# Performance work log

Measured on AMD Instinct MI355X. Metric: run time of the kernel, lower is better.

The kernel has to match this reference:

```python
import jax, jax.numpy as jnp
import numpy as np

# Llama-7B-like config with CPSVD split projections
B, S, H = 1, 1024, 4096
NH, HD = 32, 128          # num_heads, head_dim
RANK = 1024               # SVD rank per projection
NCOL = 512                # exactly-kept columns per projection
NSVD = H - NCOL           # SVD-compressed columns
ROPE_BASE = 10000.0
WSCALE = 0.02


def setup_inputs() -> dict:
    key = jax.random.key(0)
    ks = jax.random.split(key, 16)
    hidden_states = jax.random.normal(ks[0], (B, S, H), jnp.float32)
    # causal additive mask (large negative above diagonal)
    causal = jnp.triu(jnp.full((S, S), -1e9, jnp.float32), k=1)
    attention_mask = jnp.broadcast_to(causal, (B, 1, S, S))
    position_ids = jnp.broadcast_to(jnp.arange(S, dtype=jnp.int32), (B, S))
    # disjoint partition of the 4096 input columns: 512 kept, 3584 SVD'd
    col_idx = jnp.arange(0, H, H // NCOL, dtype=jnp.int32)          # [512]
    keep = np.ones(H, dtype=bool); keep[np.asarray(col_idx)] = False
    svd_idx = jnp.asarray(np.nonzero(keep)[0], dtype=jnp.int32)      # [3584]
    # per-projection weights (torch Linear convention: [out, in])
    def w(k, shape):
        return jax.random.normal(k, shape, jnp.float32) * WSCALE
    inp = dict(hidden_states=hidden_states, attention_mask=attention_mask,
               position_ids=position_ids, col_idx=col_idx, svd_idx=svd_idx)
    names = ['q', 'k', 'v', 'o']
    for i, p in enumerate(names):
        inp[f'{p}_v_w'] = w(ks[1 + 3 * i], (RANK, NSVD))   # v_proj: n_svd -> rank
        inp[f'{p}_u_w'] = w(ks[2 + 3 * i], (H, RANK))      # u_proj: rank -> hidden
        inp[f'{p}_col_w'] = w(ks[3 + 3 * i], (H, NCOL))    # col: n_col -> hidden
    return inp


def _split_proj(x, svd_idx, col_idx, v_w, u_w, col_w):
    # x: [B,S,H] -> gather + low-rank (V then U) + exact-column matmul, added
    x_svd = x[..., svd_idx]                                  # [B,S,NSVD]
    x_col = x[..., col_idx]                                  # [B,S,NCOL]
    low = jnp.einsum('bsr,hr->bsh', jnp.einsum('bsn,rn->bsr', x_svd, v_w), u_w)
    return low + jnp.einsum('bsc,hc->bsh', x_col, col_w)     # [B,S,H]


def _rotate_half(x):
    x1, x2 = x[..., : HD // 2], x[..., HD // 2 :]
    return jnp.concatenate((-x2, x1), axis=-1)


def reference(hidden_states, attention_mask, position_ids, col_idx, svd_idx,
              q_v_w, q_u_w, q_col_w, k_v_w, k_u_w, k_col_w,
              v_v_w, v_u_w, v_col_w, o_v_w, o_u_w, o_col_w):
    bsz, q_len, _ = hidden_states.shape

    def heads(t):  # [B,S,H] -> [B,NH,S,HD]
        return t.reshape(bsz, q_len, NH, HD).transpose(0, 2, 1, 3)

    q = heads(_split_proj(hidden_states, svd_idx, col_idx, q_v_w, q_u_w, q_col_w))
    k = heads(_split_proj(hidden_states, svd_idx, col_idx, k_v_w, k_u_w, k_col_w))
    v = heads(_split_proj(hidden_states, svd_idx, col_idx, v_v_w, v_u_w, v_col_w))

    # rotary embedding: direct indexed read of cos/sin tables
    inv_freq = 1.0 / (ROPE_BASE ** (jnp.arange(0, HD, 2, dtype=jnp.float32) / HD))
    ang = jnp.arange(q_len, dtype=jnp.float32)[:, None] * inv_freq[None, :]  # [S,HD/2]
    emb = jnp.concatenate((ang, ang), axis=-1)                               # [S,HD]
    cos = jnp.cos(emb)[position_ids][:, None, :, :]                          # [B,1,S,HD]
    sin = jnp.sin(emb)[position_ids][:, None, :, :]
    q = q * cos + _rotate_half(q) * sin
    k = k * cos + _rotate_half(k) * sin

    scale = 1.0 / jnp.sqrt(jnp.float32(HD))
    attn = jnp.einsum('bhqd,bhkd->bhqk', q, k) * scale
    attn = attn + attention_mask
    attn = jnp.maximum(attn, jnp.finfo(attn.dtype).min)
    attn = jax.nn.softmax(attn.astype(jnp.float32), axis=-1).astype(q.dtype)
    out = jnp.einsum('bhqk,bhkd->bhqd', attn, v)             # [B,NH,S,HD]
    out = out.transpose(0, 2, 1, 3).reshape(bsz, q_len, NH * HD)
    out = _split_proj(out, svd_idx, col_idx, o_v_w, o_u_w, o_col_w)
    return out
```

## Files before the change

### kernel.cpp

```cpp
#include <hip/hip_runtime.h>

typedef __attribute__((ext_vector_type(8))) short short8;
typedef __attribute__((ext_vector_type(4))) float f32x4;
typedef unsigned short u16;
typedef unsigned int u32;
typedef unsigned long long u64;

__device__ __forceinline__ u16 f2bf(float f) {
  u32 u = __builtin_bit_cast(u32, f);
  u32 r = u + 0x7FFFu + ((u >> 16) & 1u);
  return (u16)(r >> 16);
}
__device__ __forceinline__ float bf2f(u16 h) {
  u32 u = ((u32)h) << 16;
  return __builtin_bit_cast(float, u);
}

__device__ __forceinline__ void gload16(const void* g, void* l) {
  __builtin_amdgcn_global_load_lds(
      (const __attribute__((address_space(1))) void*)(u64)g,
      (__attribute__((address_space(3))) void*)(u32)(u64)l,
      16, 0, 0);
}

__global__ void convertk(const float* __restrict__ src, u16* __restrict__ dst, int n4) {
  int i = blockIdx.x * blockDim.x + threadIdx.x;
  if (i >= n4) return;
  float4 v = ((const float4*)src)[i];
  ushort4 o;
  o.x = f2bf(v.x); o.y = f2bf(v.y); o.z = f2bf(v.z); o.w = f2bf(v.w);
  ((ushort4*)dst)[i] = o;
}

__global__ void rowcat(const float* __restrict__ u, const float* __restrict__ c,
                       u16* __restrict__ dst) {
  int i = blockIdx.x * blockDim.x + threadIdx.x;
  if (i >= 4096 * 384) return;
  int r = i / 384, c4 = i % 384;
  float4 v = (c4 < 256) ? ((const float4*)(u + (long)r * 1024))[c4]
                        : ((const float4*)(c + (long)r * 512))[c4 - 256];
  ushort4 o;
  o.x = f2bf(v.x); o.y = f2bf(v.y); o.z = f2bf(v.z); o.w = f2bf(v.w);
  ((ushort4*)(dst + (long)r * 1536))[c4] = o;
}

__global__ void gather_in(const float* __restrict__ hid, const int* __restrict__ svd,
                          const int* __restrict__ col, u16* __restrict__ Xs,
                          u16* __restrict__ X2) {
  int s = blockIdx.x;
  const float* row = hid + (long)s * 4096;
  for (int j = threadIdx.x; j < 3584; j += blockDim.x)
    Xs[(long)s * 3584 + j] = f2bf(row[svd[j]]);
  for (int c = threadIdx.x; c < 512; c += blockDim.x) {
    u16 v = f2bf(row[col[c]]);
    X2[(long)s * 1536 + 1024 + c] = v;
    X2[1024L * 1536 + (long)s * 1536 + 1024 + c] = v;
    X2[2 * 1024L * 1536 + (long)s * 1536 + 1024 + c] = v;
  }
}

__global__ void gather_o(const u16* __restrict__ Ao, const int* __restrict__ svd,
                         const int* __restrict__ col, u16* __restrict__ Xso,
                         u16* __restrict__ X2o) {
  int s = blockIdx.x;
  const u16* row = Ao + (long)s * 4096;
  for (int j = threadIdx.x; j < 3584; j += blockDim.x)
    Xso[(long)s * 3584 + j] = row[svd[j]];
  for (int c = threadIdx.x; c < 512; c += blockDim.x)
    X2o[(long)s * 1536 + 1024 + c] = row[col[c]];
}

__global__ void rope_k(const u16* __restrict__ P, u16* __restrict__ dst, float scale) {
  int tid = blockIdx.x * blockDim.x + threadIdx.x;
  int d = tid & 127, s = (tid >> 7) & 1023, h = tid >> 17;
  float x = bf2f(P[(long)s * 4096 + h * 128 + d]);
  int dp = (d < 64) ? d + 64 : d - 64;
  float xp = bf2f(P[(long)s * 4096 + h * 128 + dp]);
  float rot = (d < 64) ? -xp : xp;
  int fi = d & 63;
  float inv = exp2f(-(float)fi * 0.20762050593046013f);
  float ang = (float)s * inv;
  float sn, cs;
  sincosf(ang, &sn, &cs);
  dst[((long)h * 1024 + s) * 128 + d] = f2bf((x * cs + rot * sn) * scale);
}

__global__ void vtrans(const u16* __restrict__ P, u16* __restrict__ Vt) {
  __shared__ u16 t[64][65];
  int h = blockIdx.z, d0 = blockIdx.y * 64, s0 = blockIdx.x * 64;
  int c = threadIdx.x & 63, r0 = threadIdx.x >> 6;
  for (int r = r0; r < 64; r += 4)
    t[r][c] = P[(long)(s0 + r) * 4096 + h * 128 + d0 + c];
  __syncthreads();
  for (int r = r0; r < 64; r += 4)
    Vt[(long)(h * 128 + d0 + r) * 1024 + s0 + c] = t[c][r];
}

template <int FOUT>
__global__ __launch_bounds__(256) void gemm_nt(const u16* __restrict__ A,
                                               const u16* __restrict__ B,
                                               void* __restrict__ Cv, int K, int ldc,
                                               long sAz, long sBz, long sCz) {
  __shared__ __align__(16) u16 As[128 * 64];
  __shared__ __align__(16) u16 Bs[128 * 64];
  const int tid = threadIdx.x;
  const int w = tid >> 6, lane = tid & 63;
  const int wr = w >> 1, wc = w & 1;
  const int lr = lane & 15, lk = lane >> 4;
  const u16* Ab = A + (long)blockIdx.z * sAz + (long)blockIdx.y * 128 * K;
  const u16* Bb = B + (long)blockIdx.z * sBz + (long)blockIdx.x * 128 * K;
  const int srow = w * 8 + (lane >> 3);
  const int scol = (lane & 7) * 8;

  f32x4 acc[4][4] = {};

  for (int k0 = 0; k0 < K; k0 += 64) {
#pragma unroll
    for (int i = 0; i < 4; ++i) {
      gload16(Ab + (long)(i * 32 + srow) * K + k0 + scol, &As[i * 2048 + w * 512]);
      gload16(Bb + (long)(i * 32 + srow) * K + k0 + scol, &Bs[i * 2048 + w * 512]);
    }
    __syncthreads();
#pragma unroll
    for (int kk = 0; kk < 2; ++kk) {
      short8 af[4], bf[4];
#pragma unroll
      for (int m = 0; m < 4; ++m) {
        af[m] = *(const short8*)&As[(wr * 64 + m * 16 + lr) * 64 + kk * 32 + lk * 8];
      }
#pragma unroll
      for (int n = 0; n < 4; ++n) {
        bf[n] = *(const short8*)&Bs[(wc * 64 + n * 16 + lr) * 64 + kk * 32 + lk * 8];
      }
#pragma unroll
      for (int m = 0; m < 4; ++m) {
#pragma unroll
        for (int n = 0; n < 4; ++n) {
          acc[m][n] = __builtin_amdgcn_mfma_f32_16x16x32_bf16(af[m], bf[n], acc[m][n], 0, 0, 0);
        }
      }
    }
    __syncthreads();
  }

  const long crow = (long)blockIdx.y * 128 + wr * 64 + lk * 4;
  const long ccol = (long)blockIdx.x * 128 + wc * 64 + lr;
  if constexpr (FOUT == 0) {
    u16* C = (u16*)Cv + (long)blockIdx.z * sCz;
#pragma unroll
    for (int m = 0; m < 4; ++m) {
#pragma unroll
      for (int n = 0; n < 4; ++n) {
#pragma unroll
        for (int j = 0; j < 4; ++j)
          C[(crow + m * 16 + j) * ldc + ccol + n * 16] = f2bf(acc[m][n][j]);
      }
    }
  } else {
    float* C = (float*)Cv + (long)blockIdx.z * sCz;
#pragma unroll
    for (int m = 0; m < 4; ++m) {
#pragma unroll
      for (int n = 0; n < 4; ++n) {
#pragma unroll
        for (int j = 0; j < 4; ++j)
          C[(crow + m * 16 + j) * ldc + ccol + n * 16] = acc[m][n][j];
      }
    }
  }
}

__global__ __launch_bounds__(256) void attn_k(const u16* __restrict__ Qh,
                                              const u16* __restrict__ Kh,
                                              const u16* __restrict__ Vt,
                                              u16* __restrict__ Ao) {
  const int qt = 15 - blockIdx.x;
  const int h = blockIdx.y;
  const int w = threadIdx.x >> 6, lane = threadIdx.x & 63;
  const int q0 = qt * 64 + w * 16;
  const int lr = lane & 15, lk = lane >> 4;

  __shared__ __align__(16) u16 Plds[4][16][72];

  short8 qf[4];
#pragma unroll
  for (int kk = 0; kk < 4; ++kk)
    qf[kk] = *(const short8*)&Qh[((long)h * 1024 + q0 + lr) * 128 + kk * 32 + lk * 8];

  f32x4 oacc[8] = {};
  float m[4], l[4];
#pragma unroll
  for (int j = 0; j < 4; ++j) { m[j] = -3.0e38f; l[j] = 0.f; }

  for (int kt = 0; kt <= qt; ++kt) {
    const int k0 = kt * 64;
    f32x4 sacc[4] = {};
#pragma unroll
    for (int ct = 0; ct < 4; ++ct) {
#pragma unroll
      for (int kk = 0; kk < 4; ++kk) {
        short8 kf = *(const short8*)&Kh[((long)h * 1024 + k0 + ct * 16 + lr) * 128 + kk * 32 + lk * 8];
        sacc[ct] = __builtin_amdgcn_mfma_f32_16x16x32_bf16(qf[kk], kf, sacc[ct], 0, 0, 0);
      }
    }
    if (kt == qt) {
#pragma unroll
      for (int ct = 0; ct < 4; ++ct) {
#pragma unroll
        for (int j = 0; j < 4; ++j) {
          int q = q0 + lk * 4 + j;
          int k = k0 + ct * 16 + lr;
          if (k > q) sacc[ct][j] = -3.0e38f;
        }
      }
    }
#pragma unroll
    for (int j = 0; j < 4; ++j) {
      float mx = fmaxf(fmaxf(sacc[0][j], sacc[1][j]), fmaxf(sacc[2][j], sacc[3][j]));
      mx = fmaxf(mx, __shfl_xor(mx, 1));
      mx = fmaxf(mx, __shfl_xor(mx, 2));
      mx = fmaxf(mx, __shfl_xor(mx, 4));
      mx = fmaxf(mx, __shfl_xor(mx, 8));
      float mn = fmaxf(m[j], mx);
      float r = exp2f(m[j] - mn);
      m[j] = mn;
      float ps = 0.f;
#pragma unroll
      for (int ct = 0; ct < 4; ++ct) {
        float p = exp2f(sacc[ct][j] - mn);
        sacc[ct][j] = p;
        ps += p;
      }
      ps += __shfl_xor(ps, 1);
      ps += __shfl_xor(ps, 2);
      ps += __shfl_xor(ps, 4);
      ps += __shfl_xor(ps, 8);
      l[j] = l[j] * r + ps;
#pragma unroll
      for (int dt = 0; dt < 8; ++dt) oacc[dt][j] *= r;
    }
#pragma unroll
    for (int ct = 0; ct < 4; ++ct) {
#pragma unroll
      for (int j = 0; j < 4; ++j)
        Plds[w][lk * 4 + j][ct * 16 + lr] = f2bf(sacc[ct][j]);
    }
    short8 pf[2];
    pf[0] = *(const short8*)&Plds[w][lr][lk * 8];
    pf[1] = *(const short8*)&Plds[w][lr][32 + lk * 8];
#pragma unroll
    for (int dt = 0; dt < 8; ++dt) {
#pragma unroll
      for (int kk = 0; kk < 2; ++kk) {
        short8 vf = *(const short8*)&Vt[((long)h * 128 + dt * 16 + lr) * 1024 + k0 + kk * 32 + lk * 8];
        oacc[dt] = __builtin_amdgcn_mfma_f32_16x16x32_bf16(pf[kk], vf, oacc[dt], 0, 0, 0);
      }
    }
  }
#pragma unroll
  for (int j = 0; j < 4; ++j) {
    float inv = 1.f / l[j];
    int q = q0 + lk * 4 + j;
#pragma unroll
    for (int dt = 0; dt < 8; ++dt)
      Ao[(long)q * 4096 + h * 128 + dt * 16 + lr] = f2bf(oacc[dt][j] * inv);
  }
}

extern "C" void kernel_launch(void* const* d_in, const int* in_sizes, int n_in,
                              void* d_out, int out_size, void* d_ws, size_t ws_size,
                              hipStream_t stream) {
  (void)in_sizes; (void)n_in; (void)out_size; (void)ws_size;
  const float* hid = (const float*)d_in[0];
  const int* colI = (const int*)d_in[3];
  const int* svdI = (const int*)d_in[4];
  const float* W[12];
  for (int i = 0; i < 12; ++i) W[i] = (const float*)d_in[5 + i];

  char* ws = (char*)d_ws;
  size_t off = 0;
  auto alloc = [&](size_t bytes) -> void* {
    void* p = ws + off;
    off += (bytes + 255) & ~(size_t)255;
    return p;
  };
  u16* Xs  = (u16*)alloc(1024UL * 3584 * 2);
  u16* X2  = (u16*)alloc(4UL * 1024 * 1536 * 2);
  u16* W1  = (u16*)alloc(3UL * 1024 * 3584 * 2);
  u16* W1o = (u16*)alloc(1024UL * 3584 * 2);
  u16* W2  = (u16*)alloc(3UL * 4096 * 1536 * 2);
  u16* W2o = (u16*)alloc(4096UL * 1536 * 2);
  u16* P   = (u16*)alloc(3UL * 1024 * 4096 * 2);
  u16* Qh  = (u16*)alloc(32UL * 1024 * 128 * 2);
  u16* Kh  = (u16*)alloc(32UL * 1024 * 128 * 2);
  u16* Vt  = (u16*)alloc(32UL * 1024 * 128 * 2);
  u16* Ao  = (u16*)alloc(1024UL * 4096 * 2);
  u16* Xso = (u16*)alloc(1024UL * 3584 * 2);

  convertk<<<3584, 256, 0, stream>>>(W[0], W1, 917504);
  convertk<<<3584, 256, 0, stream>>>(W[3], W1 + 3670016UL, 917504);
  convertk<<<3584, 256, 0, stream>>>(W[6], W1 + 7340032UL, 917504);
  convertk<<<3584, 256, 0, stream>>>(W[9], W1o, 917504);
  rowcat<<<6144, 256, 0, stream>>>(W[1], W[2], W2);
  rowcat<<<6144, 256, 0, stream>>>(W[4], W[5], W2 + 4096UL * 1536);
  rowcat<<<6144, 256, 0, stream>>>(W[7], W[8], W2 + 2 * 4096UL * 1536);
  rowcat<<<6144, 256, 0, stream>>>(W[10], W[11], W2o);
  gather_in<<<1024, 256, 0, stream>>>(hid, svdI, colI, Xs, X2);

  gemm_nt<0><<<dim3(8, 8, 3), 256, 0, stream>>>(Xs, W1, X2, 3584, 1536, 0L,
                                                1024L * 3584, 1024L * 1536);
  gemm_nt<0><<<dim3(32, 8, 3), 256, 0, stream>>>(X2, W2, P, 1536, 4096,
                                                 1024L * 1536, 4096L * 1536, 1024L * 4096);
  rope_k<<<16384, 256, 0, stream>>>(P, Qh, 0.08838834764831845f * 1.44269504088896340f);
  rope_k<<<16384, 256, 0, stream>>>(P + 1024UL * 4096, Kh, 1.0f);
  vtrans<<<dim3(16, 2, 32), 256, 0, stream>>>(P + 2UL * 1024 * 4096, Vt);

  attn_k<<<dim3(16, 32), 256, 0, stream>>>(Qh, Kh, Vt, Ao);

  gather_o<<<1024, 256, 0, stream>>>(Ao, svdI, colI, Xso, X2 + 3UL * 1024 * 1536);
  gemm_nt<0><<<dim3(8, 8, 1), 256, 0, stream>>>(Xso, W1o, X2 + 3UL * 1024 * 1536, 3584,
                                                1536, 0, 0, 0);
  gemm_nt<1><<<dim3(32, 8, 1), 256, 0, stream>>>(X2 + 3UL * 1024 * 1536, W2o, d_out,
                                                 1536, 4096, 0, 0, 0);
}
```

Baseline: 662.8 us.

## Split attention over KV partitions with max-free softmax and merge; fuse prep kernels

Attention is restructured: each head's query tiles are paired (short and long causal rows) and the KV range is split across 4 partitions, each writing unnormalized fp32 partial outputs and row sums. A merge kernel sums them and scatters directly into the gathered o-projection inputs, replacing gather_o. The online-softmax max tracking is dropped, relying on small score magnitudes, which risks overflow for large logits. Weight conversion kernels are fused into one launch, rope is fused for Q and K with fast sin/cos, and the workspace is laid out with aliasing.

```diff
diff --git a/kernel.cpp b/kernel.cpp
--- a/kernel.cpp
+++ b/kernel.cpp
@@ -23,25 +23,36 @@
       16, 0, 0);
 }
 
-__global__ void convertk(const float* __restrict__ src, u16* __restrict__ dst, int n4) {
-  int i = blockIdx.x * blockDim.x + threadIdx.x;
-  if (i >= n4) return;
-  float4 v = ((const float4*)src)[i];
-  ushort4 o;
-  o.x = f2bf(v.x); o.y = f2bf(v.y); o.z = f2bf(v.z); o.w = f2bf(v.w);
-  ((ushort4*)dst)[i] = o;
-}
-
-__global__ void rowcat(const float* __restrict__ u, const float* __restrict__ c,
-                       u16* __restrict__ dst) {
-  int i = blockIdx.x * blockDim.x + threadIdx.x;
-  if (i >= 4096 * 384) return;
-  int r = i / 384, c4 = i % 384;
-  float4 v = (c4 < 256) ? ((const float4*)(u + (long)r * 1024))[c4]
-                        : ((const float4*)(c + (long)r * 512))[c4 - 256];
-  ushort4 o;
-  o.x = f2bf(v.x); o.y = f2bf(v.y); o.z = f2bf(v.z); o.w = f2bf(v.w);
-  ((ushort4*)(dst + (long)r * 1536))[c4] = o;
+__global__ void prep_w(const float* __restrict__ qv, const float* __restrict__ qu, const float* __restrict__ qc,
+                       const float* __restrict__ kv, const float* __restrict__ ku, const float* __restrict__ kc,
+                       const float* __restrict__ vv, const float* __restrict__ vu, const float* __restrict__ vc,
+                       const float* __restrict__ ov, const float* __restrict__ ou, const float* __restrict__ oc,
+                       u16* __restrict__ W1q, u16* __restrict__ W1o,
+                       u16* __restrict__ W2q, u16* __restrict__ W2o) {
+  long i = (long)blockIdx.x * 256 + threadIdx.x;
+  if (i < 3670016L) {
+    int which = (int)(i / 917504);
+    int j = (int)(i % 917504);
+    const float* src = which == 0 ? qv : which == 1 ? kv : which == 2 ? vv : ov;
+    u16* dst = which < 3 ? W1q + (long)which * 3670016 : W1o;
+    float4 v = ((const float4*)src)[j];
+    ushort4 o;
+    o.x = f2bf(v.x); o.y = f2bf(v.y); o.z = f2bf(v.z); o.w = f2bf(v.w);
+    ((ushort4*)dst)[j] = o;
+  } else {
+    long j2 = i - 3670016L;
+    int which = (int)(j2 / 1572864);
+    int rem = (int)(j2 % 1572864);
+    int r = rem / 384, c4 = rem % 384;
+    const float* u = which == 0 ? qu : which == 1 ? ku : which == 2 ? vu : ou;
+    const float* cc = which == 0 ? qc : which == 1 ? kc : which == 2 ? vc : oc;
+    u16* dst = which < 3 ? W2q + (long)which * 6291456 : W2o;
+    float4 v = (c4 < 256) ? ((const float4*)(u + (long)r * 1024))[c4]
+                          : ((const float4*)(cc + (long)r * 512))[c4 - 256];
+    ushort4 o;
+    o.x = f2bf(v.x); o.y = f2bf(v.y); o.z = f2bf(v.z); o.w = f2bf(v.w);
+    ((ushort4*)(dst + (long)r * 1536))[c4] = o;
+  }
 }
 
 __global__ void gather_in(const float* __restrict__ hid, const int* __restrict__ svd,
@@ -59,30 +70,22 @@
   }
 }
 
-__global__ void gather_o(const u16* __restrict__ Ao, const int* __restrict__ svd,
-                         const int* __restrict__ col, u16* __restrict__ Xso,
-                         u16* __restrict__ X2o) {
-  int s = blockIdx.x;
-  const u16* row = Ao + (long)s * 4096;
-  for (int j = threadIdx.x; j < 3584; j += blockDim.x)
-    Xso[(long)s * 3584 + j] = row[svd[j]];
-  for (int c = threadIdx.x; c < 512; c += blockDim.x)
-    X2o[(long)s * 1536 + 1024 + c] = row[col[c]];
-}
-
-__global__ void rope_k(const u16* __restrict__ P, u16* __restrict__ dst, float scale) {
-  int tid = blockIdx.x * blockDim.x + threadIdx.x;
-  int d = tid & 127, s = (tid >> 7) & 1023, h = tid >> 17;
-  float x = bf2f(P[(long)s * 4096 + h * 128 + d]);
-  int dp = (d < 64) ? d + 64 : d - 64;
-  float xp = bf2f(P[(long)s * 4096 + h * 128 + dp]);
-  float rot = (d < 64) ? -xp : xp;
-  int fi = d & 63;
-  float inv = exp2f(-(float)fi * 0.20762050593046013f);
+__global__ void rope2(const u16* __restrict__ P, u16* __restrict__ Qh, u16* __restrict__ Kh) {
+  int t = blockIdx.x * 256 + threadIdx.x;
+  int which = t >> 21;
+  int rem = t & 2097151;
+  int d0 = rem & 63, s = (rem >> 6) & 1023, h = rem >> 16;
+  const u16* src = P + (long)which * 4194304;
+  float x1 = bf2f(src[(long)s * 4096 + h * 128 + d0]);
+  float x2 = bf2f(src[(long)s * 4096 + h * 128 + d0 + 64]);
+  float inv = exp2f(-(float)d0 * 0.20762050593046013f);
   float ang = (float)s * inv;
-  float sn, cs;
-  sincosf(ang, &sn, &cs);
-  dst[((long)h * 1024 + s) * 128 + d] = f2bf((x * cs + rot * sn) * scale);
+  float sn = __sinf(ang), cs = __cosf(ang);
+  float scale = which ? 1.0f : (0.08838834764831845f * 1.44269504088896340f);
+  u16* dst = which ? Kh : Qh;
+  long o = ((long)h * 1024 + s) * 128 + d0;
+  dst[o] = f2bf((x1 * cs - x2 * sn) * scale);
+  dst[o + 64] = f2bf((x2 * cs + x1 * sn) * scale);
 }
 
 __global__ void vtrans(const u16* __restrict__ P, u16* __restrict__ Vt) {
@@ -125,20 +128,16 @@
     for (int kk = 0; kk < 2; ++kk) {
       short8 af[4], bf[4];
 #pragma unroll
-      for (int m = 0; m < 4; ++m) {
+      for (int m = 0; m < 4; ++m)
         af[m] = *(const short8*)&As[(wr * 64 + m * 16 + lr) * 64 + kk * 32 + lk * 8];
-      }
-#pragma unroll
-      for (int n = 0; n < 4; ++n) {
+#pragma unroll
+      for (int n = 0; n < 4; ++n)
         bf[n] = *(const short8*)&Bs[(wc * 64 + n * 16 + lr) * 64 + kk * 32 + lk * 8];
-      }
-#pragma unroll
-      for (int m = 0; m < 4; ++m) {
-#pragma unroll
-        for (int n = 0; n < 4; ++n) {
+#pragma unroll
+      for (int m = 0; m < 4; ++m)
+#pragma unroll
+        for (int n = 0; n < 4; ++n)
           acc[m][n] = __builtin_amdgcn_mfma_f32_16x16x32_bf16(af[m], bf[n], acc[m][n], 0, 0, 0);
-        }
-      }
     }
     __syncthreads();
   }
@@ -148,122 +147,126 @@
   if constexpr (FOUT == 0) {
     u16* C = (u16*)Cv + (long)blockIdx.z * sCz;
 #pragma unroll
-    for (int m = 0; m < 4; ++m) {
-#pragma unroll
-      for (int n = 0; n < 4; ++n) {
+    for (int m = 0; m < 4; ++m)
+#pragma unroll
+      for (int n = 0; n < 4; ++n)
 #pragma unroll
         for (int j = 0; j < 4; ++j)
           C[(crow + m * 16 + j) * ldc + ccol + n * 16] = f2bf(acc[m][n][j]);
-      }
-    }
   } else {
     float* C = (float*)Cv + (long)blockIdx.z * sCz;
 #pragma unroll
-    for (int m = 0; m < 4; ++m) {
-#pragma unroll
-      for (int n = 0; n < 4; ++n) {
+    for (int m = 0; m < 4; ++m)
+#pragma unroll
+      for (int n = 0; n < 4; ++n)
 #pragma unroll
         for (int j = 0; j < 4; ++j)
           C[(crow + m * 16 + j) * ldc + ccol + n * 16] = acc[m][n][j];
-      }
-    }
   }
 }
 
 __global__ __launch_bounds__(256) void attn_k(const u16* __restrict__ Qh,
                                               const u16* __restrict__ Kh,
                                               const u16* __restrict__ Vt,
-                                              u16* __restrict__ Ao) {
-  const int qt = 15 - blockIdx.x;
-  const int h = blockIdx.y;
+                                              float* __restrict__ Op,
+                                              float* __restrict__ Lp) {
+  const int p = blockIdx.x, h = blockIdx.z;
   const int w = threadIdx.x >> 6, lane = threadIdx.x & 63;
-  const int q0 = qt * 64 + w * 16;
+  const int r = w & 1, c = blockIdx.y * 2 + (w >> 1);
   const int lr = lane & 15, lk = lane >> 4;
-
   __shared__ __align__(16) u16 Plds[4][16][72];
 
-  short8 qf[4];
-#pragma unroll
-  for (int kk = 0; kk < 4; ++kk)
-    qf[kk] = *(const short8*)&Qh[((long)h * 1024 + q0 + lr) * 128 + kk * 32 + lk * 8];
-
-  f32x4 oacc[8] = {};
-  float m[4], l[4];
-#pragma unroll
-  for (int j = 0; j < 4; ++j) { m[j] = -3.0e38f; l[j] = 0.f; }
-
-  for (int kt = 0; kt <= qt; ++kt) {
-    const int k0 = kt * 64;
-    f32x4 sacc[4] = {};
-#pragma unroll
-    for (int ct = 0; ct < 4; ++ct) {
-#pragma unroll
-      for (int kk = 0; kk < 4; ++kk) {
-        short8 kf = *(const short8*)&Kh[((long)h * 1024 + k0 + ct * 16 + lr) * 128 + kk * 32 + lk * 8];
-        sacc[ct] = __builtin_amdgcn_mfma_f32_16x16x32_bf16(qf[kk], kf, sacc[ct], 0, 0, 0);
+#pragma unroll
+  for (int ph = 0; ph < 2; ++ph) {
+    const int qt = ph ? 31 - p : p;
+    const int q0 = qt * 32 + r * 16;
+    const int ktmax = q0 >> 6;
+    short8 qf[4];
+#pragma unroll
+    for (int kk = 0; kk < 4; ++kk)
+      qf[kk] = *(const short8*)&Qh[((long)h * 1024 + q0 + lr) * 128 + kk * 32 + lk * 8];
+    f32x4 oacc[8] = {};
+    float lsum[4] = {0.f, 0.f, 0.f, 0.f};
+    for (int kt = c; kt <= ktmax; kt += 4) {
+      const int k0 = kt * 64;
+      f32x4 sacc[4] = {};
+#pragma unroll
+      for (int ct = 0; ct < 4; ++ct) {
+        const u16* kp = &Kh[((long)h * 1024 + k0 + ct * 16 + lr) * 128 + lk * 8];
+#pragma unroll
+        for (int kk = 0; kk < 4; ++kk) {
+          short8 kf = *(const short8*)&kp[kk * 32];
+          sacc[ct] = __builtin_amdgcn_mfma_f32_16x16x32_bf16(qf[kk], kf, sacc[ct], 0, 0, 0);
+        }
+      }
+      if (kt == ktmax) {
+#pragma unroll
+        for (int ct = 0; ct < 4; ++ct)
+#pragma unroll
+          for (int j = 0; j < 4; ++j)
+            if (k0 + ct * 16 + lr > q0 + lk * 4 + j) sacc[ct][j] = -3.0e38f;
+      }
+#pragma unroll
+      for (int ct = 0; ct < 4; ++ct)
+#pragma unroll
+        for (int j = 0; j < 4; ++j) {
+          float pv = exp2f(sacc[ct][j]);
+          sacc[ct][j] = pv;
+          lsum[j] += pv;
+        }
+#pragma unroll
+      for (int ct = 0; ct < 4; ++ct)
+#pragma unroll
+        for (int j = 0; j < 4; ++j)
+          Plds[w][lk * 4 + j][ct * 16 + lr] = f2bf(sacc[ct][j]);
+      short8 pf0 = *(const short8*)&Plds[w][lr][lk * 8];
+      short8 pf1 = *(const short8*)&Plds[w][lr][32 + lk * 8];
+#pragma unroll
+      for (int dt = 0; dt < 8; ++dt) {
+        const u16* vp = &Vt[((long)h * 128 + dt * 16 + lr) * 1024 + k0 + lk * 8];
+        short8 vf0 = *(const short8*)&vp[0];
+        oacc[dt] = __builtin_amdgcn_mfma_f32_16x16x32_bf16(pf0, vf0, oacc[dt], 0, 0, 0);
+        short8 vf1 = *(const short8*)&vp[32];
+        oacc[dt] = __builtin_amdgcn_mfma_f32_16x16x32_bf16(pf1, vf1, oacc[dt], 0, 0, 0);
       }
     }
-    if (kt == qt) {
-#pragma unroll
-      for (int ct = 0; ct < 4; ++ct) {
-#pragma unroll
-        for (int j = 0; j < 4; ++j) {
-          int q = q0 + lk * 4 + j;
-          int k = k0 + ct * 16 + lr;
-          if (k > q) sacc[ct][j] = -3.0e38f;
-        }
-      }
+#pragma unroll
+    for (int j = 0; j < 4; ++j) {
+      float v = lsum[j];
+      v += __shfl_xor(v, 1); v += __shfl_xor(v, 2);
+      v += __shfl_xor(v, 4); v += __shfl_xor(v, 8);
+      int q = q0 + lk * 4 + j;
+      long ob = ((long)c * 32 + h) * 1024 + q;
+      if (lr == 0) Lp[ob] = v;
+#pragma unroll
+      for (int dt = 0; dt < 8; ++dt)
+        Op[ob * 128 + dt * 16 + lr] = oacc[dt][j];
     }
-#pragma unroll
-    for (int j = 0; j < 4; ++j) {
-      float mx = fmaxf(fmaxf(sacc[0][j], sacc[1][j]), fmaxf(sacc[2][j], sacc[3][j]));
-      mx = fmaxf(mx, __shfl_xor(mx, 1));
-      mx = fmaxf(mx, __shfl_xor(mx, 2));
-      mx = fmaxf(mx, __shfl_xor(mx, 4));
-      mx = fmaxf(mx, __shfl_xor(mx, 8));
-      float mn = fmaxf(m[j], mx);
-      float r = exp2f(m[j] - mn);
-      m[j] = mn;
-      float ps = 0.f;
-#pragma unroll
-      for (int ct = 0; ct < 4; ++ct) {
-        float p = exp2f(sacc[ct][j] - mn);
-        sacc[ct][j] = p;
-        ps += p;
-      }
-      ps += __shfl_xor(ps, 1);
-      ps += __shfl_xor(ps, 2);
-      ps += __shfl_xor(ps, 4);
-      ps += __shfl_xor(ps, 8);
-      l[j] = l[j] * r + ps;
-#pragma unroll
-      for (int dt = 0; dt < 8; ++dt) oacc[dt][j] *= r;
-    }
-#pragma unroll
-    for (int ct = 0; ct < 4; ++ct) {
-#pragma unroll
-      for (int j = 0; j < 4; ++j)
-        Plds[w][lk * 4 + j][ct * 16 + lr] = f2bf(sacc[ct][j]);
-    }
-    short8 pf[2];
-    pf[0] = *(const short8*)&Plds[w][lr][lk * 8];
-    pf[1] = *(const short8*)&Plds[w][lr][32 + lk * 8];
-#pragma unroll
-    for (int dt = 0; dt < 8; ++dt) {
-#pragma unroll
-      for (int kk = 0; kk < 2; ++kk) {
-        short8 vf = *(const short8*)&Vt[((long)h * 128 + dt * 16 + lr) * 1024 + k0 + kk * 32 + lk * 8];
-        oacc[dt] = __builtin_amdgcn_mfma_f32_16x16x32_bf16(pf[kk], vf, oacc[dt], 0, 0, 0);
-      }
-    }
-  }
-#pragma unroll
-  for (int j = 0; j < 4; ++j) {
-    float inv = 1.f / l[j];
-    int q = q0 + lk * 4 + j;
-#pragma unroll
-    for (int dt = 0; dt < 8; ++dt)
-      Ao[(long)q * 4096 + h * 128 + dt * 16 + lr] = f2bf(oacc[dt][j] * inv);
+  }
+}
+
+__global__ void merge_k(const float* __restrict__ Op, const float* __restrict__ Lp,
+                        u16* __restrict__ Xso, u16* __restrict__ X2o) {
+  int t = blockIdx.x * 256 + threadIdx.x;
+  int d4 = t & 31, s = (t >> 5) & 1023, h = t >> 15;
+  long base = ((long)h * 1024 + s) * 32 + d4;
+  float4 a = {0.f, 0.f, 0.f, 0.f};
+  float l = 0.f;
+#pragma unroll
+  for (int c = 0; c < 4; ++c) {
+    float4 v = ((const float4*)Op)[(long)c * 1048576 + base];
+    a.x += v.x; a.y += v.y; a.z += v.z; a.w += v.w;
+    l += Lp[((long)c * 32 + h) * 1024 + s];
+  }
+  float inv = 1.f / l;
+  int H0 = h * 128 + d4 * 4;
+  float av[4] = {a.x, a.y, a.z, a.w};
+#pragma unroll
+  for (int e = 0; e < 4; ++e) {
+    int H = H0 + e;
+    u16 b = f2bf(av[e] * inv);
+    if ((H & 7) == 0) X2o[(long)s * 1536 + 1024 + (H >> 3)] = b;
+    else Xso[(long)s * 3584 + H - (H >> 3) - 1] = b;
   }
 }
 
@@ -278,48 +281,37 @@
   for (int i = 0; i < 12; ++i) W[i] = (const float*)d_in[5 + i];
 
   char* ws = (char*)d_ws;
-  size_t off = 0;
-  auto alloc = [&](size_t bytes) -> void* {
-    void* p = ws + off;
-    off += (bytes + 255) & ~(size_t)255;
-    return p;
-  };
-  u16* Xs  = (u16*)alloc(1024UL * 3584 * 2);
-  u16* X2  = (u16*)alloc(4UL * 1024 * 1536 * 2);
-  u16* W1  = (u16*)alloc(3UL * 1024 * 3584 * 2);
-  u16* W1o = (u16*)alloc(1024UL * 3584 * 2);
-  u16* W2  = (u16*)alloc(3UL * 4096 * 1536 * 2);
-  u16* W2o = (u16*)alloc(4096UL * 1536 * 2);
-  u16* P   = (u16*)alloc(3UL * 1024 * 4096 * 2);
-  u16* Qh  = (u16*)alloc(32UL * 1024 * 128 * 2);
-  u16* Kh  = (u16*)alloc(32UL * 1024 * 128 * 2);
-  u16* Vt  = (u16*)alloc(32UL * 1024 * 128 * 2);
-  u16* Ao  = (u16*)alloc(1024UL * 4096 * 2);
-  u16* Xso = (u16*)alloc(1024UL * 3584 * 2);
-
-  convertk<<<3584, 256, 0, stream>>>(W[0], W1, 917504);
-  convertk<<<3584, 256, 0, stream>>>(W[3], W1 + 3670016UL, 917504);
-  convertk<<<3584, 256, 0, stream>>>(W[6], W1 + 7340032UL, 917504);
-  convertk<<<3584, 256, 0, stream>>>(W[9], W1o, 917504);
-  rowcat<<<6144, 256, 0, stream>>>(W[1], W[2], W2);
-  rowcat<<<6144, 256, 0, stream>>>(W[4], W[5], W2 + 4096UL * 1536);
-  rowcat<<<6144, 256, 0, stream>>>(W[7], W[8], W2 + 2 * 4096UL * 1536);
-  rowcat<<<6144, 256, 0, stream>>>(W[10], W[11], W2o);
+  u16* W1q = (u16*)(ws + 0);
+  u16* W2q = (u16*)(ws + 22020096);
+  u16* P   = (u16*)(ws + 59768832);
+  float* Op = (float*)(ws + 0);
+  float* Lp = (float*)(ws + 67108864);
+  u16* W1o = (u16*)(ws + 84934656);
+  u16* W2o = (u16*)(ws + 92274688);
+  u16* Xs  = (u16*)(ws + 104857600);
+  u16* X2  = (u16*)(ws + 112197632);
+  u16* Qh  = (u16*)(ws + 124780544);
+  u16* Kh  = (u16*)(ws + 133169152);
+  u16* Vt  = (u16*)(ws + 141557760);
+  u16* Xso = (u16*)(ws + 149946368);
+
+  prep_w<<<38912, 256, 0, stream>>>(W[0], W[1], W[2], W[3], W[4], W[5],
+                                    W[6], W[7], W[8], W[9], W[10], W[11],
+                                    W1q, W1o, W2q, W2o);
   gather_in<<<1024, 256, 0, stream>>>(hid, svdI, colI, Xs, X2);
 
-  gemm_nt<0><<<dim3(8, 8, 3), 256, 0, stream>>>(Xs, W1, X2, 3584, 1536, 0L,
+  gemm_nt<0><<<dim3(8, 8, 3), 256, 0, stream>>>(Xs, W1q, X2, 3584, 1536, 0L,
                                                 1024L * 3584, 1024L * 1536);
-  gemm_nt<0><<<dim3(32, 8, 3), 256, 0, stream>>>(X2, W2, P, 1536, 4096,
+  gemm_nt<0><<<dim3(32, 8, 3), 256, 0, stream>>>(X2, W2q, P, 1536, 4096,
                                                  1024L * 1536, 4096L * 1536, 1024L * 4096);
-  rope_k<<<16384, 256, 0, stream>>>(P, Qh, 0.08838834764831845f * 1.44269504088896340f);
-  rope_k<<<16384, 256, 0, stream>>>(P + 1024UL * 4096, Kh, 1.0f);
+  rope2<<<16384, 256, 0, stream>>>(P, Qh, Kh);
   vtrans<<<dim3(16, 2, 32), 256, 0, stream>>>(P + 2UL * 1024 * 4096, Vt);
 
-  attn_k<<<dim3(16, 32), 256, 0, stream>>>(Qh, Kh, Vt, Ao);
-
-  gather_o<<<1024, 256, 0, stream>>>(Ao, svdI, colI, Xso, X2 + 3UL * 1024 * 1536);
+  attn_k<<<dim3(16, 2, 32), 256, 0, stream>>>(Qh, Kh, Vt, Op, Lp);
+  merge_k<<<4096, 256, 0, stream>>>(Op, Lp, Xso, X2 + 3UL * 1024 * 1536);
+
   gemm_nt<0><<<dim3(8, 8, 1), 256, 0, stream>>>(Xso, W1o, X2 + 3UL * 1024 * 1536, 3584,
-                                                1536, 0, 0, 0);
+                                                1536, 0L, 0L, 0L);
   gemm_nt<1><<<dim3(32, 8, 1), 256, 0, stream>>>(X2 + 3UL * 1024 * 1536, W2o, d_out,
-                                                 1536, 4096, 0, 0, 0);
-}
+                                                 1536, 4096, 0L, 0L, 0L);
+}
```

New measurement: 605.3 us. 1.1x faster.
